# Performance work log

Measured on AMD Instinct MI355X. Metric: run time of the kernel, lower is better.

## Reference

```python
import jax, jax.numpy as jnp
import numpy as np

RES = 32          # resolution (32, 32) -> N = 1024 tokens
HEADS = 16
EMB = 1024
BATCH = 8
N = RES * RES


def _bias_idxs(res):
    # relative-offset index table, [N, N] with values in [0, res*res)
    coords = np.stack(np.meshgrid(np.arange(res), np.arange(res), indexing='ij'), -1).reshape(-1, 2)
    d = np.abs(coords[:, None, :] - coords[None, :, :])  # [N, N, 2]
    return jnp.asarray(d[..., 0] * res + d[..., 1], dtype=jnp.int64)


def setup_inputs() -> dict:
    key = jax.random.key(0)
    k1, k2, k3, k4, k5 = jax.random.split(key, 5)
    x = jax.random.normal(k1, (BATCH, N, EMB), dtype=jnp.float32)
    w_qkv = jax.random.normal(k2, (3 * EMB, EMB), dtype=jnp.float32) * 0.02
    biases = jax.random.normal(k3, (HEADS, RES * RES), dtype=jnp.float32) * 0.02
    bias_idxs = _bias_idxs(RES)
    w_out = jax.random.normal(k4, (EMB, EMB), dtype=jnp.float32) * 0.02
    b_out = jax.random.normal(k5, (EMB,), dtype=jnp.float32) * 0.02
    return {"x": x, "w_qkv": w_qkv, "biases": biases,
            "bias_idxs": bias_idxs, "w_out": w_out, "b_out": b_out}


def reference(x, w_qkv, biases, bias_idxs, w_out, b_out):
    b, n, e = x.shape
    h = HEADS
    d = e // h
    scale = d ** -0.5
    # to_qkv: Linear(e, 3e, bias=False); torch Linear computes x @ W.T
    qkv = x @ w_qkv.T                                   # [b, n, 3e]
    q, k, v = jnp.split(qkv, 3, axis=-1)
    def to_heads(t):
        return t.reshape(b, n, h, d).transpose(0, 2, 1, 3)  # b h n d
    q, k, v = to_heads(q), to_heads(k), to_heads(v)
    scores = jnp.einsum('bhid,bhjd->bhij', q, k) * scale    # [b, h, n, n]
    scores = scores + biases[:, bias_idxs]                  # gather -> [h, n, n], broadcast over b
    attn = jax.nn.softmax(scores, axis=-1)
    out = jnp.einsum('bhij,bhjd->bhid', attn, v)            # [b, h, n, d]
    out = out.transpose(0, 2, 1, 3).reshape(b, n, e)        # b n (h d)
    # to_out: Linear(e, e) with bias (dropout = identity at inference)
    return out @ w_out.T + b_out
```

## Files before the change

### kernel.cpp

```cpp
#include <hip/hip_runtime.h>
#include <stdint.h>


#define LOG2E 1.4426950408889634f

typedef __attribute__((ext_vector_type(8))) short short8;
typedef __attribute__((ext_vector_type(4))) short short4v;
typedef __attribute__((ext_vector_type(4))) float floatx4;
typedef __attribute__((ext_vector_type(2))) unsigned int uint2v;

__device__ __forceinline__ short f2bf(float f) {
  uint32_t u = __builtin_bit_cast(uint32_t, f);
  u = (u + 0x7FFFu + ((u >> 16) & 1u)) >> 16;
  return (short)(uint16_t)u;
}
__device__ __forceinline__ float bf2f(short s) {
  uint32_t u = ((uint32_t)(uint16_t)s) << 16;
  return __builtin_bit_cast(float, u);
}
__device__ __forceinline__ float fast_exp2(float x) {
#if __has_builtin(__builtin_amdgcn_exp2f)
  return __builtin_amdgcn_exp2f(x);
#else
  return exp2f(x);
#endif
}

__device__ __forceinline__ void gload_lds16(const short* g, short* l) {
  __builtin_amdgcn_global_load_lds(
      (const __attribute__((address_space(1))) void*)g,
      (__attribute__((address_space(3))) void*)l, 16, 0, 0);
}

__global__ void cvt_bf16(const float* __restrict__ src, short* __restrict__ dst, int n4) {
  int i = blockIdx.x * 256 + threadIdx.x;
  if (i >= n4) return;
  float4 f = ((const float4*)src)[i];
  short4v o;
  o.x = f2bf(f.x); o.y = f2bf(f.y); o.z = f2bf(f.z); o.w = f2bf(f.w);
  ((short4v*)dst)[i] = o;
}

__global__ void bias_precomp(const float* __restrict__ biases, short* __restrict__ biast) {
  int t = blockIdx.x * 256 + threadIdx.x;
  int lane = t & 63;
  int tile = t >> 6;
  int jt = tile & 63, it = (tile >> 6) & 63, h = tile >> 12;
  int i0 = it * 16 + ((lane >> 4) << 2);
  int j = jt * 16 + (lane & 15);
  int rj = j >> 5, cj = j & 31;
  short4v o;
#pragma unroll
  for (int r = 0; r < 4; r++) {
    int i = i0 + r;
    int ri = i >> 5, ci = i & 31;
    int dr = ri - rj; if (dr < 0) dr = -dr;
    int dc = ci - cj; if (dc < 0) dc = -dc;
    o[r] = f2bf(biases[h * 1024 + dr * 32 + dc] * LOG2E);
  }
  *(short4v*)&biast[(size_t)t * 4] = o;
}

template <int MODE>
__global__ __launch_bounds__(256, 2) void gemm_bt(
    const short* __restrict__ A, const short* __restrict__ Bt,
    short* __restrict__ qo, short* __restrict__ ko, short* __restrict__ vto,
    const float* __restrict__ bvec, float* __restrict__ outf) {
  __shared__ __align__(16) short sA[128 * 64];
  __shared__ __align__(16) short sB[128 * 64];
  const int tid = threadIdx.x;
  const int w = tid >> 6, lane = tid & 63;
  const int wr = w >> 1, wc = w & 1;
  const int bm = blockIdx.y, bn = blockIdx.x;
  const int qd = lane >> 4, col = lane & 15;

  floatx4 acc[4][4] = {};
  const int rowA0 = bm * 128, rowB0 = bn * 128;
  const int ciw = w * 256;

  for (int kk = 0; kk < 1024; kk += 64) {
    __syncthreads();
#pragma unroll
    for (int n = 0; n < 4; n++) {
      int ci = ciw + n * 64 + lane;
      int r = ci >> 3, c = (ci & 7) ^ (r & 7);
      gload_lds16(A + (size_t)(rowA0 + r) * 1024 + kk + c * 8, &sA[ci * 8]);
    }
#pragma unroll
    for (int n = 0; n < 4; n++) {
      int ci = ciw + n * 64 + lane;
      int r = ci >> 3, c = (ci & 7) ^ (r & 7);
      gload_lds16(Bt + (size_t)(rowB0 + r) * 1024 + kk + c * 8, &sB[ci * 8]);
    }
    __syncthreads();

#pragma unroll
    for (int ks = 0; ks < 2; ks++) {
      const int ch = qd + ks * 4;
      short8 af[4], bff[4];
#pragma unroll
      for (int rt = 0; rt < 4; rt++) {
        int r = wr * 64 + rt * 16 + col;
        af[rt] = *(const short8*)&sA[r * 64 + ((ch ^ (r & 7)) << 3)];
      }
#pragma unroll
      for (int ct = 0; ct < 4; ct++) {
        int r = wc * 64 + ct * 16 + col;
        bff[ct] = *(const short8*)&sB[r * 64 + ((ch ^ (r & 7)) << 3)];
      }
#pragma unroll
      for (int rt = 0; rt < 4; rt++)
#pragma unroll
        for (int ct = 0; ct < 4; ct++)
          acc[rt][ct] = __builtin_amdgcn_mfma_f32_16x16x32_bf16(af[rt], bff[ct], acc[rt][ct], 0, 0, 0);
    }
  }

  if (MODE == 0) {
    if (bn >= 16) {
#pragma unroll
      for (int rt = 0; rt < 4; rt++) {
#pragma unroll
        for (int ct = 0; ct < 4; ct++) {
          int Cg = bn * 128 + wc * 64 + ct * 16 + col;
          int e = Cg & 1023, h = e >> 6, dd = e & 63;
          short4v pv;
#pragma unroll
          for (int r = 0; r < 4; r++) pv[r] = f2bf(acc[rt][ct][r]);
          int R0 = bm * 128 + wr * 64 + rt * 16 + qd * 4;
          int b = R0 >> 10, n0 = R0 & 1023;
          int bh = b * 16 + h;
          *(short4v*)&vto[((size_t)bh * 64 + dd) * 1024 + n0] = pv;
        }
      }
    } else {
#pragma unroll
      for (int rt = 0; rt < 4; rt++) {
#pragma unroll
        for (int ct = 0; ct < 4; ct++) {
          int Cg = bn * 128 + wc * 64 + ct * 16 + col;
          int which = Cg >> 10, e = Cg & 1023, h = e >> 6, dd = e & 63;
#pragma unroll
          for (int r = 0; r < 4; r++) {
            int R = bm * 128 + wr * 64 + rt * 16 + qd * 4 + r;
            int b = R >> 10, n = R & 1023;
            int bh = b * 16 + h;
            short v = f2bf(acc[rt][ct][r]);
            if (which == 0)
              qo[((size_t)bh * 1024 + n) * 64 + dd] = v;
            else
              ko[((size_t)bh * 1024 + n) * 64 + dd] = v;
          }
        }
      }
    }
  } else {
#pragma unroll
    for (int rt = 0; rt < 4; rt++)
#pragma unroll
      for (int ct = 0; ct < 4; ct++) {
        int Cg = bn * 128 + wc * 64 + ct * 16 + col;
        float bo = bvec[Cg];
#pragma unroll
        for (int r = 0; r < 4; r++) {
          int R = bm * 128 + wr * 64 + rt * 16 + qd * 4 + r;
          outf[(size_t)R * 1024 + Cg] = acc[rt][ct][r] + bo;
        }
      }
  }
}

__global__ __launch_bounds__(256, 2) void attn_fused(
    const short* __restrict__ q, const short* __restrict__ k,
    const short* __restrict__ vt, const short* __restrict__ biast,
    short* __restrict__ ao) {
  __shared__ __align__(16) short sK[2][128 * 64];
  __shared__ __align__(16) short sV[2][64 * 128];
  __shared__ __align__(16) short sP[64 * 128];
  const int tid = threadIdx.x, w = tid >> 6, lane = tid & 63;
  const int bh = blockIdx.x, qt = blockIdx.y;
  const int h = bh & 15;
  const int qd = lane >> 4, col = lane & 15;
  const short* qb = q + (size_t)bh * 65536;
  const short* kb = k + (size_t)bh * 65536;
  const short* vb = vt + (size_t)bh * 65536;
  const int ciw = w * 256;

#pragma unroll
  for (int n = 0; n < 2; n++) {
    int ci = w * 128 + n * 64 + lane;
    int r = ci >> 3, c = (ci & 7) ^ (r & 7);
    gload_lds16(qb + (size_t)(qt * 64 + r) * 64 + c * 8, &sP[ci * 8]);
  }
#pragma unroll
  for (int n = 0; n < 4; n++) {
    int ci = ciw + n * 64 + lane;
    int r = ci >> 3, c = (ci & 7) ^ (r & 7);
    gload_lds16(kb + (size_t)r * 64 + c * 8, &sK[0][ci * 8]);
  }
#pragma unroll
  for (int n = 0; n < 4; n++) {
    int ci = ciw + n * 64 + lane;
    int r = ci >> 4, c = (ci & 15) ^ (r & 15);
    gload_lds16(vb + (size_t)r * 1024 + c * 8, &sV[0][ci * 8]);
  }
  __syncthreads();
  short8 bq[2][4];
#pragma unroll
  for (int ks = 0; ks < 2; ks++) {
    const int ch = qd + ks * 4;
#pragma unroll
    for (int ct = 0; ct < 4; ct++) {
      int r2 = ct * 16 + col;
      bq[ks][ct] = *(const short8*)&sP[r2 * 64 + ((ch ^ (r2 & 7)) << 3)];
    }
  }

  short8 onesf;
#pragma unroll
  for (int t = 0; t < 8; t++) onesf[t] = (short)0x3F80;

  floatx4 oacc[4] = {};
  floatx4 osum = {};
  const float SCL = 0.125f * LOG2E;

  for (int js = 0; js < 8; js++) {
    const int cur = js & 1, nxt = cur ^ 1;
    __syncthreads();
    if (js < 7) {
#pragma unroll
      for (int n = 0; n < 4; n++) {
        int ci = ciw + n * 64 + lane;
        int r = ci >> 3, c = (ci & 7) ^ (r & 7);
        gload_lds16(kb + (size_t)((js + 1) * 128 + r) * 64 + c * 8, &sK[nxt][ci * 8]);
      }
#pragma unroll
      for (int n = 0; n < 4; n++) {
        int ci = ciw + n * 64 + lane;
        int r = ci >> 4, c = (ci & 15) ^ (r & 15);
        gload_lds16(vb + (size_t)r * 1024 + (js + 1) * 128 + c * 8, &sV[nxt][ci * 8]);
      }
    }

    const short* sKc = sK[cur];
#pragma unroll
    for (int rt = 0; rt < 2; rt++) {
      const int a = js * 8 + w * 2 + rt;
      const int s = w * 8 + rt * 4 + qd;
      short4v bfrag[4];
#pragma unroll
      for (int ct = 0; ct < 4; ct++) {
        int b = qt * 4 + ct;
        bfrag[ct] = *(const short4v*)&biast[((((size_t)h * 64 + a) * 64 + b) << 8) + lane * 4];
      }
      const int r = w * 32 + rt * 16 + col;
      short8 ak0 = *(const short8*)&sKc[r * 64 + (((qd + 0) ^ (r & 7)) << 3)];
      short8 ak1 = *(const short8*)&sKc[r * 64 + (((qd + 4) ^ (r & 7)) << 3)];
      floatx4 sacc[4] = {};
#pragma unroll
      for (int ct = 0; ct < 4; ct++)
        sacc[ct] = __builtin_amdgcn_mfma_f32_16x16x32_bf16(ak0, bq[0][ct], sacc[ct], 0, 0, 0);
#pragma unroll
      for (int ct = 0; ct < 4; ct++)
        sacc[ct] = __builtin_amdgcn_mfma_f32_16x16x32_bf16(ak1, bq[1][ct], sacc[ct], 0, 0, 0);
#pragma unroll
      for (int ct = 0; ct < 4; ct++) {
        int i = ct * 16 + col;
        float e0 = fast_exp2(fmaf(sacc[ct][0], SCL, bf2f(bfrag[ct][0])));
        float e1 = fast_exp2(fmaf(sacc[ct][1], SCL, bf2f(bfrag[ct][1])));
        float e2 = fast_exp2(fmaf(sacc[ct][2], SCL, bf2f(bfrag[ct][2])));
        float e3 = fast_exp2(fmaf(sacc[ct][3], SCL, bf2f(bfrag[ct][3])));
        uint32_t u0 = __builtin_bit_cast(uint32_t, e0) + 0x8000u;
        uint32_t u1 = __builtin_bit_cast(uint32_t, e1) + 0x8000u;
        uint32_t u2 = __builtin_bit_cast(uint32_t, e2) + 0x8000u;
        uint32_t u3 = __builtin_bit_cast(uint32_t, e3) + 0x8000u;
        uint2v pk;
        pk.x = __builtin_amdgcn_perm(u1, u0, 0x07060302u);
        pk.y = __builtin_amdgcn_perm(u3, u2, 0x07060302u);
        *(uint2v*)&sP[i * 128 + ((s ^ (i & 15)) << 2)] = pk;
      }
    }
    __syncthreads();

    const short* sVc = sV[cur];
#pragma unroll
    for (int ks = 0; ks < 4; ks++) {
      const int ch = ks * 4 + qd;
      int m = w * 16 + col;
      short4v lo = *(const short4v*)&sP[m * 128 + (((2 * ch) ^ col) << 2)];
      short4v hi = *(const short4v*)&sP[m * 128 + (((2 * ch + 1) ^ col) << 2)];
      short8 ap = __builtin_shufflevector(lo, hi, 0, 1, 2, 3, 4, 5, 6, 7);
      short8 bv[4];
#pragma unroll
      for (int ct = 0; ct < 4; ct++) {
        int d = ct * 16 + col;
        bv[ct] = *(const short8*)&sVc[d * 128 + ((ch ^ (d & 15)) << 3)];
      }
#pragma unroll
      for (int ct = 0; ct < 4; ct++)
        oacc[ct] = __builtin_amdgcn_mfma_f32_16x16x32_bf16(ap, bv[ct], oacc[ct], 0, 0, 0);
      osum = __builtin_amdgcn_mfma_f32_16x16x32_bf16(ap, onesf, osum, 0, 0, 0);
    }
  }

  const int b = bh >> 4;
  floatx4 inv;
#pragma unroll
  for (int r = 0; r < 4; r++) inv[r] = 1.0f / osum[r];
#pragma unroll
  for (int ct = 0; ct < 4; ct++)
#pragma unroll
    for (int r = 0; r < 4; r++) {
      int n = qt * 64 + w * 16 + qd * 4 + r;
      int dd = ct * 16 + col;
      ao[(((size_t)b * 1024 + n) << 10) + h * 64 + dd] = f2bf(oacc[ct][r] * inv[r]);
    }
}

extern "C" void kernel_launch(void* const* d_in, const int* in_sizes, int n_in,
                              void* d_out, int out_size, void* d_ws, size_t ws_size,
                              hipStream_t stream) {
  const float* x = (const float*)d_in[0];
  const float* w_qkv = (const float*)d_in[1];
  const float* biases = (const float*)d_in[2];
  const float* w_out = (const float*)d_in[4];
  const float* b_out = (const float*)d_in[5];
  float* out = (float*)d_out;

  char* ws = (char*)d_ws;
  short* xb    = (short*)(ws + 0);
  short* wqkvb = (short*)(ws + 16777216);
  short* woutb = (short*)(ws + 23068672);
  short* qb    = (short*)(ws + 25165824);
  short* kb    = (short*)(ws + 41943040);
  short* vtb   = (short*)(ws + 58720256);
  short* aob   = (short*)(ws + 75497472);
  short* biast = (short*)(ws + 92274688);

  cvt_bf16<<<8192, 256, 0, stream>>>(x, xb, 8192 * 1024 / 4);
  cvt_bf16<<<3072, 256, 0, stream>>>(w_qkv, wqkvb, 3072 * 1024 / 4);
  cvt_bf16<<<1024, 256, 0, stream>>>(w_out, woutb, 1024 * 1024 / 4);
  bias_precomp<<<16384, 256, 0, stream>>>(biases, biast);

  gemm_bt<0><<<dim3(24, 64), 256, 0, stream>>>(xb, wqkvb, qb, kb, vtb, nullptr, nullptr);
  attn_fused<<<dim3(128, 16), 256, 0, stream>>>(qb, kb, vtb, biast, aob);
  gemm_bt<1><<<dim3(8, 64), 256, 0, stream>>>(aob, woutb, nullptr, nullptr, nullptr, b_out, out);
}
```

Baseline: 268.5 us.

## Compress bias table via Toeplitz structure, fuse prep kernels, single-buffer attention LDS

Merges the three bf16 conversion launches and the bias precompute into one prep kernel. The bias table shrinks from a full per-head N×N gather (16M entries) to a compact table indexed by row-block distance, relying on the separable |dr|,|dc| structure, so the attention kernel reads a much smaller, cache-friendly bias array. Attention drops K/V double buffering to cut LDS use and raise the occupancy target to 3 blocks per CU. In exchange, K/V loads are no longer overlapped with compute and need an extra barrier per iteration.

```diff
diff --git a/kernel.cpp b/kernel.cpp
--- a/kernel.cpp
+++ b/kernel.cpp
@@ -32,33 +32,36 @@
       (__attribute__((address_space(3))) void*)l, 16, 0, 0);
 }
 
-__global__ void cvt_bf16(const float* __restrict__ src, short* __restrict__ dst, int n4) {
-  int i = blockIdx.x * 256 + threadIdx.x;
-  if (i >= n4) return;
-  float4 f = ((const float4*)src)[i];
-  short4v o;
-  o.x = f2bf(f.x); o.y = f2bf(f.y); o.z = f2bf(f.z); o.w = f2bf(f.w);
-  ((short4v*)dst)[i] = o;
-}
-
-__global__ void bias_precomp(const float* __restrict__ biases, short* __restrict__ biast) {
-  int t = blockIdx.x * 256 + threadIdx.x;
-  int lane = t & 63;
-  int tile = t >> 6;
-  int jt = tile & 63, it = (tile >> 6) & 63, h = tile >> 12;
-  int i0 = it * 16 + ((lane >> 4) << 2);
-  int j = jt * 16 + (lane & 15);
-  int rj = j >> 5, cj = j & 31;
-  short4v o;
-#pragma unroll
-  for (int r = 0; r < 4; r++) {
-    int i = i0 + r;
-    int ri = i >> 5, ci = i & 31;
-    int dr = ri - rj; if (dr < 0) dr = -dr;
-    int dc = ci - cj; if (dc < 0) dc = -dc;
-    o[r] = f2bf(biases[h * 1024 + dr * 32 + dc] * LOG2E);
-  }
-  *(short4v*)&biast[(size_t)t * 4] = o;
+__global__ void prep(const float* __restrict__ x, const float* __restrict__ wqkv,
+                     const float* __restrict__ wout, const float* __restrict__ biases,
+                     short* __restrict__ xb, short* __restrict__ wqkvb,
+                     short* __restrict__ woutb, short* __restrict__ biast) {
+  int blk = blockIdx.x, tid = threadIdx.x;
+  if (blk < 12288) {
+    const float* src;
+    short* dst;
+    int i;
+    if (blk < 8192) { src = x; dst = xb; i = blk * 256 + tid; }
+    else if (blk < 11264) { src = wqkv; dst = wqkvb; i = (blk - 8192) * 256 + tid; }
+    else { src = wout; dst = woutb; i = (blk - 11264) * 256 + tid; }
+    float4 f = ((const float4*)src)[i];
+    short4v o;
+    o.x = f2bf(f.x); o.y = f2bf(f.y); o.z = f2bf(f.z); o.w = f2bf(f.w);
+    ((short4v*)dst)[i] = o;
+  } else {
+    int tile = (blk - 12288) * 4 + (tid >> 6);
+    int lane = tid & 63, qd = lane >> 4, col = lane & 15;
+    int bp = tile & 1, ap = (tile >> 1) & 1, dra = (tile >> 2) & 31, h = tile >> 7;
+    int ci = 16 * bp + col;
+    short4v o;
+#pragma unroll
+    for (int r = 0; r < 4; r++) {
+      int cj = 16 * ap + 4 * qd + r;
+      int dc = cj - ci; if (dc < 0) dc = -dc;
+      o[r] = f2bf(biases[h * 1024 + dra * 32 + dc] * LOG2E);
+    }
+    *(short4v*)&biast[(size_t)tile * 256 + lane * 4] = o;
+  }
 }
 
 template <int MODE>
@@ -170,12 +173,12 @@
   }
 }
 
-__global__ __launch_bounds__(256, 2) void attn_fused(
+__global__ __launch_bounds__(256, 3) void attn_fused(
     const short* __restrict__ q, const short* __restrict__ k,
     const short* __restrict__ vt, const short* __restrict__ biast,
     short* __restrict__ ao) {
-  __shared__ __align__(16) short sK[2][128 * 64];
-  __shared__ __align__(16) short sV[2][64 * 128];
+  __shared__ __align__(16) short sK[128 * 64];
+  __shared__ __align__(16) short sVt[64 * 128];
   __shared__ __align__(16) short sP[64 * 128];
   const int tid = threadIdx.x, w = tid >> 6, lane = tid & 63;
   const int bh = blockIdx.x, qt = blockIdx.y;
@@ -192,18 +195,6 @@
     int r = ci >> 3, c = (ci & 7) ^ (r & 7);
     gload_lds16(qb + (size_t)(qt * 64 + r) * 64 + c * 8, &sP[ci * 8]);
   }
-#pragma unroll
-  for (int n = 0; n < 4; n++) {
-    int ci = ciw + n * 64 + lane;
-    int r = ci >> 3, c = (ci & 7) ^ (r & 7);
-    gload_lds16(kb + (size_t)r * 64 + c * 8, &sK[0][ci * 8]);
-  }
-#pragma unroll
-  for (int n = 0; n < 4; n++) {
-    int ci = ciw + n * 64 + lane;
-    int r = ci >> 4, c = (ci & 15) ^ (r & 15);
-    gload_lds16(vb + (size_t)r * 1024 + c * 8, &sV[0][ci * 8]);
-  }
   __syncthreads();
   short8 bq[2][4];
 #pragma unroll
@@ -225,37 +216,37 @@
   const float SCL = 0.125f * LOG2E;
 
   for (int js = 0; js < 8; js++) {
-    const int cur = js & 1, nxt = cur ^ 1;
-    __syncthreads();
-    if (js < 7) {
-#pragma unroll
-      for (int n = 0; n < 4; n++) {
-        int ci = ciw + n * 64 + lane;
-        int r = ci >> 3, c = (ci & 7) ^ (r & 7);
-        gload_lds16(kb + (size_t)((js + 1) * 128 + r) * 64 + c * 8, &sK[nxt][ci * 8]);
-      }
-#pragma unroll
-      for (int n = 0; n < 4; n++) {
-        int ci = ciw + n * 64 + lane;
-        int r = ci >> 4, c = (ci & 15) ^ (r & 15);
-        gload_lds16(vb + (size_t)r * 1024 + (js + 1) * 128 + c * 8, &sV[nxt][ci * 8]);
-      }
-    }
-
-    const short* sKc = sK[cur];
+    __syncthreads();
+#pragma unroll
+    for (int n = 0; n < 4; n++) {
+      int ci = ciw + n * 64 + lane;
+      int r = ci >> 3, c = (ci & 7) ^ (r & 7);
+      gload_lds16(kb + (size_t)(js * 128 + r) * 64 + c * 8, &sK[ci * 8]);
+    }
+#pragma unroll
+    for (int n = 0; n < 4; n++) {
+      int ci = ciw + n * 64 + lane;
+      int r = ci >> 4, c = (ci & 15) ^ (r & 15);
+      gload_lds16(vb + (size_t)r * 1024 + js * 128 + c * 8, &sVt[ci * 8]);
+    }
+    __syncthreads();
+
 #pragma unroll
     for (int rt = 0; rt < 2; rt++) {
       const int a = js * 8 + w * 2 + rt;
       const int s = w * 8 + rt * 4 + qd;
+      const int ar = a >> 1, ap = a & 1;
       short4v bfrag[4];
 #pragma unroll
       for (int ct = 0; ct < 4; ct++) {
         int b = qt * 4 + ct;
-        bfrag[ct] = *(const short4v*)&biast[((((size_t)h * 64 + a) * 64 + b) << 8) + lane * 4];
+        int dra = ar - (b >> 1); if (dra < 0) dra = -dra;
+        int tile = ((h * 32 + dra) * 2 + ap) * 2 + (b & 1);
+        bfrag[ct] = *(const short4v*)&biast[(size_t)tile * 256 + lane * 4];
       }
       const int r = w * 32 + rt * 16 + col;
-      short8 ak0 = *(const short8*)&sKc[r * 64 + (((qd + 0) ^ (r & 7)) << 3)];
-      short8 ak1 = *(const short8*)&sKc[r * 64 + (((qd + 4) ^ (r & 7)) << 3)];
+      short8 ak0 = *(const short8*)&sK[r * 64 + (((qd + 0) ^ (r & 7)) << 3)];
+      short8 ak1 = *(const short8*)&sK[r * 64 + (((qd + 4) ^ (r & 7)) << 3)];
       floatx4 sacc[4] = {};
 #pragma unroll
       for (int ct = 0; ct < 4; ct++)
@@ -282,7 +273,6 @@
     }
     __syncthreads();
 
-    const short* sVc = sV[cur];
 #pragma unroll
     for (int ks = 0; ks < 4; ks++) {
       const int ch = ks * 4 + qd;
@@ -294,7 +284,7 @@
 #pragma unroll
       for (int ct = 0; ct < 4; ct++) {
         int d = ct * 16 + col;
-        bv[ct] = *(const short8*)&sVc[d * 128 + ((ch ^ (d & 15)) << 3)];
+        bv[ct] = *(const short8*)&sVt[d * 128 + ((ch ^ (d & 15)) << 3)];
       }
 #pragma unroll
       for (int ct = 0; ct < 4; ct++)
@@ -337,11 +327,7 @@
   short* aob   = (short*)(ws + 75497472);
   short* biast = (short*)(ws + 92274688);
 
-  cvt_bf16<<<8192, 256, 0, stream>>>(x, xb, 8192 * 1024 / 4);
-  cvt_bf16<<<3072, 256, 0, stream>>>(w_qkv, wqkvb, 3072 * 1024 / 4);
-  cvt_bf16<<<1024, 256, 0, stream>>>(w_out, woutb, 1024 * 1024 / 4);
-  bias_precomp<<<16384, 256, 0, stream>>>(biases, biast);
-
+  prep<<<13312, 256, 0, stream>>>(x, w_qkv, w_out, biases, xb, wqkvb, woutb, biast);
   gemm_bt<0><<<dim3(24, 64), 256, 0, stream>>>(xb, wqkvb, qb, kb, vtb, nullptr, nullptr);
   attn_fused<<<dim3(128, 16), 256, 0, stream>>>(qb, kb, vtb, biast, aob);
   gemm_bt<1><<<dim3(8, 64), 256, 0, stream>>>(aob, woutb, nullptr, nullptr, nullptr, b_out, out);
```

Result: faster. 238.0 us (-11.4%).
